# Kernel tuning notes

Hardware: AMD Instinct MI355X
Metric: run time of the kernel (lower is better)

The kernel has to match this reference:

```python
import jax, jax.numpy as jnp
import numpy as np

B, D, N, H = 1024, 512, 16, 512  # batch, latent, branches, hidden


def _lrelu(v):
    return jnp.where(v >= 0, v, 0.1 * v)  # LeakyReLU(0.1)


def setup_inputs() -> dict:
    key = jax.random.key(0)
    ks = jax.random.split(key, 9)
    s = 0.02
    return {
        "x": jax.random.normal(ks[0], (B, D, N), dtype=jnp.float32),
        "Ws1": jax.random.normal(ks[1], (D, D), dtype=jnp.float32) * s,
        "bs1": jnp.zeros((D,), dtype=jnp.float32),
        "Ws2": jax.random.normal(ks[2], (D, D), dtype=jnp.float32) * s,
        "bs2": jnp.zeros((D,), dtype=jnp.float32),
        # per-branch binary classifiers: Linear(D,H)+LeakyReLU+Linear(H,1)
        "Wc1": jax.random.normal(ks[3], (N, D, H), dtype=jnp.float32) * s,
        "bc1": jnp.zeros((N, H), dtype=jnp.float32),
        "Wc2": jax.random.normal(ks[4], (N, H), dtype=jnp.float32) * s,
        "bc2": jnp.zeros((N,), dtype=jnp.float32),
    }


def reference(x, Ws1, bs1, Ws2, bs2, Wc1, bc1, Wc2, bc2):
    # x: [B, D, N] -> per-branch tokens [B, N, D]
    xb = jnp.transpose(x, (0, 2, 1))
    # shared MLP applied to every branch slice (same weights)
    h = _lrelu(xb @ Ws1 + bs1)
    shared = _lrelu(h @ Ws2 + bs2)  # [B, N, D]
    # per-branch classifier on its own branch slice -> sigmoid probs
    h1 = _lrelu(jnp.einsum('bnd,ndh->bnh', shared, Wc1) + bc1)
    logits = jnp.einsum('bnh,nh->bn', h1, Wc2) + bc2  # [B, N]
    out = jax.nn.sigmoid(logits)[:, None, :]  # [B, 1, N]
    # full pass: concat branch slices along batch (branch-major), every
    # classifier applied to the full stack -> raw logits
    full_in = jnp.transpose(shared, (1, 0, 2)).reshape(N * B, D)  # [M, D]
    h2 = _lrelu(jnp.einsum('md,ndh->mnh', full_in, Wc1) + bc1)  # [M, N, H]
    full_logits = jnp.einsum('mnh,nh->mn', h2, Wc2) + bc2  # [M, N]
    full_out = full_logits[:, None, :]  # [N*B, 1, N]
    return (out, full_out)
```

## Files before the change

### kernel.cpp

```cpp
#include <hip/hip_runtime.h>
#include <hip/hip_bf16.h>
#include <stdint.h>

#define Bq 1024
#define Dq 512
#define Nq 16
#define Hq 512
#define Mq (Bq*Nq)

typedef short v8s  __attribute__((ext_vector_type(8)));
typedef float v16f __attribute__((ext_vector_type(16)));

typedef __attribute__((address_space(3))) unsigned int as3_u32;
typedef __attribute__((address_space(1))) const unsigned int as1_u32;

__device__ __forceinline__ unsigned short f2bf(float f) {
  union { float f; unsigned u; } v; v.f = f;
  return (unsigned short)((v.u + 0x7fffu + ((v.u >> 16) & 1u)) >> 16);
}

__global__ void k_transpose_x(const float* __restrict__ x, unsigned short* __restrict__ xb) {
  __shared__ float lds[Dq][Nq + 1];
  const int b = blockIdx.x;
  const float* xi = x + (size_t)b * Dq * Nq;
  const int t = threadIdx.x;
  for (int p = 0; p < (Dq*Nq)/256; ++p) {
    int i = t + p*256;
    lds[i >> 4][i & (Nq-1)] = xi[i];
  }
  __syncthreads();
  unsigned short* o = xb + (size_t)b * Nq * Dq;
  for (int p = 0; p < (Dq*Nq)/256; ++p) {
    int i = t + p*256;
    o[i] = f2bf(lds[i & (Dq-1)][i >> 9]);
  }
}

__global__ void k_transpose_w(const float* __restrict__ Ws1, const float* __restrict__ Ws2,
                              const float* __restrict__ Wc1,
                              unsigned short* __restrict__ Ws1t, unsigned short* __restrict__ Ws2t,
                              unsigned short* __restrict__ Wc1t) {
  __shared__ float tile[32][33];
  const int z = blockIdx.z;
  const float* in;
  unsigned short* out;
  if (z == 0)      { in = Ws1; out = Ws1t; }
  else if (z == 1) { in = Ws2; out = Ws2t; }
  else             { in = Wc1 + (size_t)(z-2) * 512 * 512; out = Wc1t + (size_t)(z-2) * 512 * 512; }
  const int tx = threadIdx.x, ty = threadIdx.y;
  const int c0 = blockIdx.x * 32, r0 = blockIdx.y * 32;
#pragma unroll
  for (int j = 0; j < 4; ++j)
    tile[ty + j*8][tx] = in[(size_t)(r0 + ty + j*8) * 512 + c0 + tx];
  __syncthreads();
#pragma unroll
  for (int j = 0; j < 4; ++j) {
    int c = c0 + ty + j*8;
    int r = r0 + tx;
    out[(size_t)c * 512 + r] = f2bf(tile[tx][ty + j*8]);
  }
}

template<int MODE, int BM>
__global__ __launch_bounds__(256, 2)
void k_gemm(const unsigned short* __restrict__ A,
            const unsigned short* __restrict__ Bt,
            const float* __restrict__ bias,
            void* __restrict__ out_,
            const float* __restrict__ w2,
            int permute) {
  constexpr int BN = 128, BK = 32, KD = 512;
  constexpr int NI = (BM == 256) ? 4 : 2;
  constexpr int AG = BM / 16;
  constexpr int TG = AG + BN / 16;
  __shared__ __align__(16) unsigned short As[2][BM][BK];
  __shared__ __align__(16) unsigned short Bs[2][BN][BK];

  const int t = threadIdx.x;
  const int wave = t >> 6, lane = t & 63;
  const int wr = (BM == 256) ? wave : (wave >> 1);
  const int wc = (BM == 256) ? 0    : (wave & 1);
  const int l32 = lane & 31, kh0 = lane >> 5;
  const int bm = blockIdx.x * BM, bn = blockIdx.y * BN;
  const int z = blockIdx.z;

  const unsigned short* Bz = Bt + (size_t)z * KD * 512;
  const float* biasz = bias + (size_t)z * 512;

  const int lrow = lane >> 2;
  const int lslot = lane & 3;

  auto stage = [&](int buf, int kt) {
#pragma unroll
    for (int i = wave; i < TG; i += 4) {
      const int isA = (i < AG);
      const int r0 = (isA ? i : i - AG) * 16;
      const int row = r0 + lrow;
      const int cg = lslot ^ ((row >> 1) & 3);
      const unsigned short* g = isA ? &A [(size_t)(bm + row) * KD + kt*BK + cg*8]
                                    : &Bz[(size_t)(bn + row) * KD + kt*BK + cg*8];
      as3_u32* d = isA ? (as3_u32*)&As[buf][r0][0] : (as3_u32*)&Bs[buf][r0][0];
      __builtin_amdgcn_global_load_lds((as1_u32*)g, d, 16, 0, 0);
    }
  };

  v16f acc[2][NI] = {};

  stage(0, 0);
  __syncthreads();

  for (int kt = 0; kt < KD / BK; ++kt) {
    const int cur = kt & 1;
    if (kt + 1 < KD / BK) stage(cur ^ 1, kt + 1);

    v8s af[2][2], bf[NI][2];
#pragma unroll
    for (int mi = 0; mi < 2; ++mi) {
      int ra = wr*64 + mi*32 + l32;
#pragma unroll
      for (int kh = 0; kh < 2; ++kh) {
        int c = kh*2 + kh0;
        af[mi][kh] = *(const v8s*)&As[cur][ra][(c ^ ((ra >> 1) & 3)) * 8];
      }
    }
#pragma unroll
    for (int ni = 0; ni < NI; ++ni) {
      int rb = wc*64 + ni*32 + l32;
#pragma unroll
      for (int kh = 0; kh < 2; ++kh) {
        int c = kh*2 + kh0;
        bf[ni][kh] = *(const v8s*)&Bs[cur][rb][(c ^ ((rb >> 1) & 3)) * 8];
      }
    }
#pragma unroll
    for (int kh = 0; kh < 2; ++kh)
#pragma unroll
      for (int mi = 0; mi < 2; ++mi)
#pragma unroll
        for (int ni = 0; ni < NI; ++ni)
          acc[mi][ni] = __builtin_amdgcn_mfma_f32_32x32x16_bf16(af[mi][kh], bf[ni][kh], acc[mi][ni], 0, 0, 0);
    __syncthreads();
  }

  if (MODE == 0) {
    unsigned short* O = (unsigned short*)out_;
#pragma unroll
    for (int mi = 0; mi < 2; ++mi) {
#pragma unroll
      for (int ni = 0; ni < NI; ++ni) {
        int col = bn + wc*64 + ni*32 + l32;
        float bcol = biasz[col];
#pragma unroll
        for (int reg = 0; reg < 16; ++reg) {
          int rl = (reg & 3) + 8*(reg >> 2) + 4*kh0;
          int grow = bm + wr*64 + mi*32 + rl;
          int orow = permute ? ((grow & 15) * Bq + (grow >> 4)) : grow;
          float v = acc[mi][ni][reg] + bcol;
          v = v >= 0.f ? v : 0.1f * v;
          O[(size_t)orow * 512 + col] = f2bf(v);
        }
      }
    }
  } else {
    float* FL = (float*)out_;
    const float* w2z = w2 + (size_t)z * 512;
#pragma unroll
    for (int mi = 0; mi < 2; ++mi) {
#pragma unroll
      for (int reg = 0; reg < 16; ++reg) {
        int rl = (reg & 3) + 8*(reg >> 2) + 4*kh0;
        float s = 0.f;
#pragma unroll
        for (int ni = 0; ni < NI; ++ni) {
          int col = bn + ni*32 + l32;
          float v = acc[mi][ni][reg] + biasz[col];
          v = v >= 0.f ? v : 0.1f * v;
          s += v * w2z[col];
        }
#pragma unroll
        for (int off = 1; off < 32; off <<= 1)
          s += __shfl_xor(s, off, 64);
        if (l32 == 0) {
          int grow = bm + wave*64 + mi*32 + rl;
          atomicAdd(&FL[(size_t)grow * Nq + z], s);
        }
      }
    }
  }
}

__global__ void k_final(const float* __restrict__ fl, const float* __restrict__ bc2,
                        float* __restrict__ out) {
  int i = blockIdx.x * 256 + threadIdx.x;
  int m = i >> 4, n = i & 15;
  float v = fl[i] + bc2[n];
  out[Mq + i] = v;
  if (n == (m >> 10)) {
    int b = m & (Bq - 1);
    out[b * Nq + n] = 1.f / (1.f + __expf(-v));
  }
}

extern "C" void kernel_launch(void* const* d_in, const int* in_sizes, int n_in,
                              void* d_out, int out_size, void* d_ws, size_t ws_size,
                              hipStream_t stream) {
  (void)in_sizes; (void)n_in; (void)out_size; (void)ws_size;
  const float* x   = (const float*)d_in[0];
  const float* Ws1 = (const float*)d_in[1];
  const float* bs1 = (const float*)d_in[2];
  const float* Ws2 = (const float*)d_in[3];
  const float* bs2 = (const float*)d_in[4];
  const float* Wc1 = (const float*)d_in[5];
  const float* bc1 = (const float*)d_in[6];
  const float* Wc2 = (const float*)d_in[7];
  const float* bc2 = (const float*)d_in[8];

  char* ws = (char*)d_ws;
  unsigned short* Xb   = (unsigned short*)(ws);
  unsigned short* Hbuf = (unsigned short*)(ws + (size_t)16*1024*1024);
  unsigned short* Sm   = (unsigned short*)(ws + (size_t)32*1024*1024);
  unsigned short* Ws1t = (unsigned short*)(ws + (size_t)48*1024*1024);
  unsigned short* Ws2t = (unsigned short*)(ws + (size_t)48*1024*1024 + 512*1024);
  unsigned short* Wc1t = (unsigned short*)(ws + (size_t)49*1024*1024);
  float*          FL   = (float*)         (ws + (size_t)57*1024*1024);

  hipMemsetAsync(FL, 0, (size_t)Mq * Nq * sizeof(float), stream);

  k_transpose_x<<<Bq, 256, 0, stream>>>(x, Xb);
  k_transpose_w<<<dim3(16,16,18), dim3(32,8), 0, stream>>>(Ws1, Ws2, Wc1, Ws1t, Ws2t, Wc1t);

  k_gemm<0,128><<<dim3(128,4,1), 256, 0, stream>>>(Xb,   Ws1t, bs1, Hbuf, nullptr, 0);
  k_gemm<0,128><<<dim3(128,4,1), 256, 0, stream>>>(Hbuf, Ws2t, bs2, Sm,   nullptr, 1);
  k_gemm<1,256><<<dim3(64,4,16), 256, 0, stream>>>(Sm, Wc1t, bc1, FL, Wc2, 0);

  k_final<<<(Mq*Nq)/256, 256, 0, stream>>>(FL, bc2, (float*)d_out);
}
```

Measured before the change: 342.4 us.

## Add 256x256 head GEMM kernel with 8 waves and fine-grained LDS pipelining

Replaces the dominant head GEMM (16 branches x 16384 rows x 512 x 512) with a new kernel that uses 512 threads and 256x256 output tiles. Global-to-LDS loads are split into half-K stages interleaved between MFMA groups, with explicit vmcnt waits, raw barriers, sched_barrier and s_setprio to keep loads in flight during compute. The larger tile halves the number of B-column blocks, so fewer atomics into FL and less operand refetch. The risks are higher register and LDS pressure (128 KB LDS with launch bounds of 2 blocks per CU) and fragile manual wait counts.

```diff
diff --git a/kernel.cpp b/kernel.cpp
--- a/kernel.cpp
+++ b/kernel.cpp
@@ -13,6 +13,8 @@
 
 typedef __attribute__((address_space(3))) unsigned int as3_u32;
 typedef __attribute__((address_space(1))) const unsigned int as1_u32;
+
+#define VMCNT(n) asm volatile("s_waitcnt vmcnt(" #n ")" ::: "memory")
 
 __device__ __forceinline__ unsigned short f2bf(float f) {
   union { float f; unsigned u; } v; v.f = f;
@@ -189,6 +191,136 @@
   }
 }
 
+__global__ __launch_bounds__(512, 2)
+void k_headgemm(const unsigned short* __restrict__ A,
+                const unsigned short* __restrict__ Bt,
+                const float* __restrict__ bias,
+                float* __restrict__ FL,
+                const float* __restrict__ w2) {
+  __shared__ __align__(16) unsigned short sm[2][2][2][256][32];
+
+  const int t = threadIdx.x;
+  const int wave = t >> 6, lane = t & 63;
+  const int wr = wave >> 2, wc = wave & 3;
+  const int l32 = lane & 31, kh0 = lane >> 5;
+  const int bm = blockIdx.x * 256, bn = blockIdx.y * 256;
+  const int z = blockIdx.z;
+
+  const unsigned short* Bz = Bt + (size_t)z * Dq * 512;
+  const float* biasz = bias + (size_t)z * 512;
+  const float* w2z   = w2   + (size_t)z * 512;
+
+  const int srow = wave*16 + (lane >> 2);
+  const int sgc  = (lane & 3) ^ ((srow >> 1) & 3);
+  const unsigned short* aSrc = A  + (size_t)(bm + srow) * Dq + sgc*8;
+  const unsigned short* bSrc = Bz + (size_t)(bn + srow) * Dq + sgc*8;
+
+  auto stageA = [&](int T, int h) {
+    const int buf = T & 1;
+    const unsigned short* g = aSrc + T*64 + h*32;
+#pragma unroll
+    for (int part = 0; part < 2; ++part) {
+      as3_u32* d = (as3_u32*)&sm[buf][h][0][part*128 + wave*16][0];
+      __builtin_amdgcn_global_load_lds((as1_u32*)(g + (size_t)part*128*Dq), d, 16, 0, 0);
+    }
+  };
+  auto stageB = [&](int T, int h) {
+    const int buf = T & 1;
+    const unsigned short* g = bSrc + T*64 + h*32;
+#pragma unroll
+    for (int part = 0; part < 2; ++part) {
+      as3_u32* d = (as3_u32*)&sm[buf][h][1][part*128 + wave*16][0];
+      __builtin_amdgcn_global_load_lds((as1_u32*)(g + (size_t)part*128*Dq), d, 16, 0, 0);
+    }
+  };
+
+  int offA[4][2], offB[2][2];
+#pragma unroll
+  for (int mi = 0; mi < 4; ++mi) {
+    int r = wr*128 + mi*32 + l32;
+#pragma unroll
+    for (int par = 0; par < 2; ++par)
+      offA[mi][par] = r*64 + (((par*2 + kh0) ^ ((r >> 1) & 3)) * 16);
+  }
+#pragma unroll
+  for (int ni = 0; ni < 2; ++ni) {
+    int r = wc*64 + ni*32 + l32;
+#pragma unroll
+    for (int par = 0; par < 2; ++par)
+      offB[ni][par] = r*64 + (((par*2 + kh0) ^ ((r >> 1) & 3)) * 16);
+  }
+
+  v16f acc[4][2] = {};
+
+  stageA(0, 0); stageB(0, 0);
+  stageA(0, 1); stageB(0, 1);
+  stageA(1, 0); stageB(1, 0);
+  VMCNT(8);
+  __builtin_amdgcn_s_barrier();
+
+  for (int tt = 0; tt < 8; ++tt) {
+    const int buf = tt & 1;
+#pragma unroll
+    for (int q = 0; q < 4; ++q) {
+      const int h = q >> 1, par = q & 1;
+      const char* baseA = (const char*)&sm[buf][h][0][0][0];
+      const char* baseB = (const char*)&sm[buf][h][1][0][0];
+      v8s af[4], bf[2];
+#pragma unroll
+      for (int mi = 0; mi < 4; ++mi) af[mi] = *(const v8s*)(baseA + offA[mi][par]);
+#pragma unroll
+      for (int ni = 0; ni < 2; ++ni) bf[ni] = *(const v8s*)(baseB + offB[ni][par]);
+
+      if      (q == 0) { if (tt + 1 < 8) stageA(tt + 1, 1); }
+      else if (q == 1) { if (tt + 1 < 8) stageB(tt + 1, 1); }
+      else if (q == 2) { if (tt + 2 < 8) stageA(tt + 2, 0); }
+      else             { if (tt + 2 < 8) stageB(tt + 2, 0); }
+
+      __builtin_amdgcn_s_barrier();
+
+      __builtin_amdgcn_s_setprio(1);
+#pragma unroll
+      for (int mi = 0; mi < 4; ++mi)
+#pragma unroll
+        for (int ni = 0; ni < 2; ++ni)
+          acc[mi][ni] = __builtin_amdgcn_mfma_f32_32x32x16_bf16(af[mi], bf[ni], acc[mi][ni], 0, 0, 0);
+      __builtin_amdgcn_s_setprio(0);
+
+      if (q == 1) {
+        if (tt < 7) { VMCNT(8); } else { VMCNT(0); }
+      } else if (q == 3) {
+        if (tt < 6)       { VMCNT(8); }
+        else if (tt == 6) { VMCNT(4); }
+      }
+      __builtin_amdgcn_s_barrier();
+      __builtin_amdgcn_sched_barrier(0);
+    }
+  }
+
+#pragma unroll
+  for (int mi = 0; mi < 4; ++mi) {
+#pragma unroll
+    for (int reg = 0; reg < 16; ++reg) {
+      int rl = (reg & 3) + 8*(reg >> 2) + 4*kh0;
+      float s = 0.f;
+#pragma unroll
+      for (int ni = 0; ni < 2; ++ni) {
+        int col = bn + wc*64 + ni*32 + l32;
+        float v = acc[mi][ni][reg] + biasz[col];
+        v = v >= 0.f ? v : 0.1f * v;
+        s += v * w2z[col];
+      }
+#pragma unroll
+      for (int off = 1; off < 32; off <<= 1)
+        s += __shfl_xor(s, off, 64);
+      if (l32 == 0) {
+        int grow = bm + wr*128 + mi*32 + rl;
+        atomicAdd(&FL[(size_t)grow * Nq + z], s);
+      }
+    }
+  }
+}
+
 __global__ void k_final(const float* __restrict__ fl, const float* __restrict__ bc2,
                         float* __restrict__ out) {
   int i = blockIdx.x * 256 + threadIdx.x;
@@ -231,7 +363,7 @@
 
   k_gemm<0,128><<<dim3(128,4,1), 256, 0, stream>>>(Xb,   Ws1t, bs1, Hbuf, nullptr, 0);
   k_gemm<0,128><<<dim3(128,4,1), 256, 0, stream>>>(Hbuf, Ws2t, bs2, Sm,   nullptr, 1);
-  k_gemm<1,256><<<dim3(64,4,16), 256, 0, stream>>>(Sm, Wc1t, bc1, FL, Wc2, 0);
+  k_headgemm<<<dim3(64,2,16), 512, 0, stream>>>(Sm, Wc1t, bc1, FL, Wc2);
 
   k_final<<<(Mq*Nq)/256, 256, 0, stream>>>(FL, bc2, (float*)d_out);
 }
```

New measurement: 405.9 us. 18.6% more time.

## Replace head GEMM with 256x256-tile 8-wave pipelined MFMA kernel

Applied to the files above, without the earlier changes.

Adds a dedicated head GEMM kernel with 256x256 output tiles, 512 threads and 16x16x32 bf16 MFMAs. It stages K in 64-wide double-buffered halves with direct global-to-LDS loads, manual vmcnt waits, s_barrier phases and setprio around MFMA bursts, so loads overlap compute. The larger tile halves the number of N-blocks, which reduces redundant A reads and atomic adds per row. In exchange it needs 128 KB of LDS per block and heavy accumulator register use, which may limit occupancy, and the hand-written sync is fragile.

```diff
diff --git a/kernel.cpp b/kernel.cpp
--- a/kernel.cpp
+++ b/kernel.cpp
@@ -9,10 +9,13 @@
 #define Mq (Bq*Nq)
 
 typedef short v8s  __attribute__((ext_vector_type(8)));
+typedef float v4f  __attribute__((ext_vector_type(4)));
 typedef float v16f __attribute__((ext_vector_type(16)));
 
 typedef __attribute__((address_space(3))) unsigned int as3_u32;
 typedef __attribute__((address_space(1))) const unsigned int as1_u32;
+
+#define VMCNT(n) asm volatile("s_waitcnt vmcnt(" #n ")" ::: "memory")
 
 __device__ __forceinline__ unsigned short f2bf(float f) {
   union { float f; unsigned u; } v; v.f = f;
@@ -189,6 +192,149 @@
   }
 }
 
+__global__ __launch_bounds__(512, 2)
+void k_headgemm(const unsigned short* __restrict__ A,
+                const unsigned short* __restrict__ Bt,
+                const float* __restrict__ bias,
+                float* __restrict__ FL,
+                const float* __restrict__ w2) {
+  __shared__ __align__(16) unsigned short sm[2][2][2][256][32];
+
+  const int t = threadIdx.x;
+  const int wave = t >> 6, lane = t & 63;
+  const int wr = wave >> 2, wc = wave & 3;
+  const int bm = blockIdx.x * 256, bn = blockIdx.y * 256;
+  const int z = blockIdx.z;
+
+  const unsigned short* Bz = Bt + (size_t)z * Dq * 512;
+  const float* biasz = bias + (size_t)z * 512;
+  const float* w2z   = w2   + (size_t)z * 512;
+
+  const int sr = lane >> 2;
+  const int sc = (lane & 3) ^ ((sr >> 1) & 3);
+  const unsigned short* aSrc = A  + (size_t)(bm + wave*32 + sr) * Dq + sc*8;
+  const unsigned short* bSrc = Bz + (size_t)(bn + wave*32 + sr) * Dq + sc*8;
+
+  auto stage = [&](int T, int h, int op) {
+    const unsigned short* src = (op == 0 ? aSrc : bSrc) + T*64 + h*32;
+#pragma unroll
+    for (int j = 0; j < 2; ++j) {
+      as3_u32* d = (as3_u32*)&sm[T & 1][h][op][wave*32 + j*16][0];
+      __builtin_amdgcn_global_load_lds((as1_u32*)(src + (size_t)j*16*Dq), d, 16, 0, 0);
+    }
+  };
+
+  const int fr = lane & 15, fq = lane >> 4;
+  const int swz = ((fq ^ ((fr >> 1) & 3)) * 16);
+  const int offA0 = (wr*128 + fr) * 64 + swz;
+  const int offB0 = (wc*64  + fr) * 64 + swz;
+
+  v4f acc[8][4] = {};
+
+  stage(0, 0, 0); stage(0, 0, 1);
+  stage(0, 1, 0); stage(0, 1, 1);
+  VMCNT(4);
+  __builtin_amdgcn_s_barrier();
+  __builtin_amdgcn_sched_barrier(0);
+
+#pragma unroll 2
+  for (int tt = 0; tt < 8; ++tt) {
+    const char* bA0 = (const char*)&sm[tt & 1][0][0][0][0];
+    const char* bB0 = (const char*)&sm[tt & 1][0][1][0][0];
+    const char* bA1 = (const char*)&sm[tt & 1][1][0][0][0];
+    const char* bB1 = (const char*)&sm[tt & 1][1][1][0][0];
+    v8s af[4], bf[4];
+
+#pragma unroll
+    for (int i = 0; i < 4; ++i) af[i] = *(const v8s*)(bA0 + offA0 + i*1024);
+#pragma unroll
+    for (int i = 0; i < 4; ++i) bf[i] = *(const v8s*)(bB0 + offB0 + i*1024);
+    if (tt + 1 < 8) stage(tt + 1, 0, 0);
+    __builtin_amdgcn_s_barrier();
+    __builtin_amdgcn_s_setprio(1);
+#pragma unroll
+    for (int mi = 0; mi < 4; ++mi)
+#pragma unroll
+      for (int ni = 0; ni < 4; ++ni)
+        acc[mi][ni] = __builtin_amdgcn_mfma_f32_16x16x32_bf16(af[mi], bf[ni], acc[mi][ni], 0, 0, 0);
+    __builtin_amdgcn_s_setprio(0);
+    __builtin_amdgcn_s_barrier();
+
+#pragma unroll
+    for (int i = 0; i < 4; ++i) af[i] = *(const v8s*)(bA0 + offA0 + (4 + i)*1024);
+    if (tt + 1 < 8) stage(tt + 1, 0, 1);
+    __builtin_amdgcn_s_barrier();
+    __builtin_amdgcn_s_setprio(1);
+#pragma unroll
+    for (int mi = 0; mi < 4; ++mi)
+#pragma unroll
+      for (int ni = 0; ni < 4; ++ni)
+        acc[4 + mi][ni] = __builtin_amdgcn_mfma_f32_16x16x32_bf16(af[mi], bf[ni], acc[4 + mi][ni], 0, 0, 0);
+    __builtin_amdgcn_s_setprio(0);
+    if (tt < 7) { VMCNT(4); } else { VMCNT(0); }
+    __builtin_amdgcn_s_barrier();
+    __builtin_amdgcn_sched_barrier(0);
+
+#pragma unroll
+    for (int i = 0; i < 4; ++i) af[i] = *(const v8s*)(bA1 + offA0 + i*1024);
+#pragma unroll
+    for (int i = 0; i < 4; ++i) bf[i] = *(const v8s*)(bB1 + offB0 + i*1024);
+    if (tt + 1 < 8) stage(tt + 1, 1, 0);
+    __builtin_amdgcn_s_barrier();
+    __builtin_amdgcn_s_setprio(1);
+#pragma unroll
+    for (int mi = 0; mi < 4; ++mi)
+#pragma unroll
+      for (int ni = 0; ni < 4; ++ni)
+        acc[mi][ni] = __builtin_amdgcn_mfma_f32_16x16x32_bf16(af[mi], bf[ni], acc[mi][ni], 0, 0, 0);
+    __builtin_amdgcn_s_setprio(0);
+    __builtin_amdgcn_s_barrier();
+
+#pragma unroll
+    for (int i = 0; i < 4; ++i) af[i] = *(const v8s*)(bA1 + offA0 + (4 + i)*1024);
+    if (tt + 1 < 8) stage(tt + 1, 1, 1);
+    __builtin_amdgcn_s_barrier();
+    __builtin_amdgcn_s_setprio(1);
+#pragma unroll
+    for (int mi = 0; mi < 4; ++mi)
+#pragma unroll
+      for (int ni = 0; ni < 4; ++ni)
+        acc[4 + mi][ni] = __builtin_amdgcn_mfma_f32_16x16x32_bf16(af[mi], bf[ni], acc[4 + mi][ni], 0, 0, 0);
+    __builtin_amdgcn_s_setprio(0);
+    if (tt < 7) { VMCNT(4); }
+    __builtin_amdgcn_s_barrier();
+    __builtin_amdgcn_sched_barrier(0);
+  }
+
+  float bcol[4], wcol[4];
+#pragma unroll
+  for (int ni = 0; ni < 4; ++ni) {
+    int col = bn + wc*64 + ni*16 + fr;
+    bcol[ni] = biasz[col];
+    wcol[ni] = w2z[col];
+  }
+#pragma unroll
+  for (int mi = 0; mi < 8; ++mi) {
+#pragma unroll
+    for (int reg = 0; reg < 4; ++reg) {
+      float s = 0.f;
+#pragma unroll
+      for (int ni = 0; ni < 4; ++ni) {
+        float v = acc[mi][ni][reg] + bcol[ni];
+        v = v >= 0.f ? v : 0.1f * v;
+        s += v * wcol[ni];
+      }
+#pragma unroll
+      for (int off = 1; off < 16; off <<= 1)
+        s += __shfl_xor(s, off, 64);
+      if (fr == 0) {
+        int grow = bm + wr*128 + mi*16 + fq*4 + reg;
+        atomicAdd(&FL[(size_t)grow * Nq + z], s);
+      }
+    }
+  }
+}
+
 __global__ void k_final(const float* __restrict__ fl, const float* __restrict__ bc2,
                         float* __restrict__ out) {
   int i = blockIdx.x * 256 + threadIdx.x;
@@ -231,7 +377,7 @@
 
   k_gemm<0,128><<<dim3(128,4,1), 256, 0, stream>>>(Xb,   Ws1t, bs1, Hbuf, nullptr, 0);
   k_gemm<0,128><<<dim3(128,4,1), 256, 0, stream>>>(Hbuf, Ws2t, bs2, Sm,   nullptr, 1);
-  k_gemm<1,256><<<dim3(64,4,16), 256, 0, stream>>>(Sm, Wc1t, bc1, FL, Wc2, 0);
+  k_headgemm<<<dim3(64,2,16), 512, 0, stream>>>(Sm, Wc1t, bc1, FL, Wc2);
 
   k_final<<<(Mq*Nq)/256, 256, 0, stream>>>(FL, bc2, (float*)d_out);
 }
```

New measurement: 334.5 us. -2.3%, faster.

## Replace head GEMM with triple-buffered 16x16 MFMA kernel and XCD-aware block mapping

Applied to the files above, without the earlier changes.

Adds a dedicated kernel for the dominant per-branch head GEMM. It uses 128x128 tiles, a three-stage LDS ring filled by global_load_lds with explicit vmcnt waits and raw s_barrier, 16x16x32 bf16 MFMA with a 4x4 per-wave fragment, and s_setprio around the MFMA block. Blocks are linearised with a stride-8 remap so blocks that share weight and activation tiles land on the same XCD. The goal is to hide global latency better and raise occupancy compared with the double-buffered 256-row kernel. In exchange it issues more atomicAdds per output row, and the hand-placed wait counts must stay exactly right.

```diff
diff --git a/kernel.cpp b/kernel.cpp
--- a/kernel.cpp
+++ b/kernel.cpp
@@ -9,10 +9,13 @@
 #define Mq (Bq*Nq)
 
 typedef short v8s  __attribute__((ext_vector_type(8)));
+typedef float v4f  __attribute__((ext_vector_type(4)));
 typedef float v16f __attribute__((ext_vector_type(16)));
 
 typedef __attribute__((address_space(3))) unsigned int as3_u32;
 typedef __attribute__((address_space(1))) const unsigned int as1_u32;
+
+#define VMCNT(n) asm volatile("s_waitcnt vmcnt(" #n ")" ::: "memory")
 
 __device__ __forceinline__ unsigned short f2bf(float f) {
   union { float f; unsigned u; } v; v.f = f;
@@ -189,6 +192,122 @@
   }
 }
 
+__global__ __launch_bounds__(256, 3)
+void k_headgemm(const unsigned short* __restrict__ A,
+                const unsigned short* __restrict__ Bt,
+                const float* __restrict__ bias,
+                float* __restrict__ FL,
+                const float* __restrict__ w2) {
+  __shared__ __align__(16) unsigned short As[3][128][32];
+  __shared__ __align__(16) unsigned short Bs[3][128][32];
+
+  const int t = threadIdx.x;
+  const int wave = t >> 6, lane = t & 63;
+  const int wr = wave >> 1, wc = wave & 1;
+  const int fr = lane & 15, fq = lane >> 4;
+
+  const int bid = blockIdx.x;
+  const int lin = (bid & 7) * 1024 + (bid >> 3);
+  const int bm = (lin & 127) * 128;
+  const int bn = ((lin >> 7) & 3) * 128;
+  const int z  = lin >> 9;
+
+  const unsigned short* Bz = Bt + (size_t)z * Dq * 512;
+  const float* biasz = bias + (size_t)z * 512;
+  const float* w2z   = w2   + (size_t)z * 512;
+
+  const int sr = lane >> 2;
+  const int sc = (lane & 3) ^ ((sr >> 1) & 3);
+  const unsigned short* aSrc = A  + (size_t)(bm + wave*32 + sr) * Dq + sc*8;
+  const unsigned short* bSrc = Bz + (size_t)(bn + wave*32 + sr) * Dq + sc*8;
+  char* dstA = (char*)As + (wave*32) * 64;
+  char* dstB = (char*)Bs + (wave*32) * 64;
+
+  auto stage = [&](int T, int slot) {
+    if (T >= 16) return;
+#pragma unroll
+    for (int j = 0; j < 2; ++j) {
+      __builtin_amdgcn_global_load_lds((as1_u32*)(aSrc + T*32 + (size_t)j*16*Dq),
+                                       (as3_u32*)(dstA + slot*8192 + j*1024), 16, 0, 0);
+      __builtin_amdgcn_global_load_lds((as1_u32*)(bSrc + T*32 + (size_t)j*16*Dq),
+                                       (as3_u32*)(dstB + slot*8192 + j*1024), 16, 0, 0);
+    }
+  };
+
+  const int swz = (fq ^ ((fr >> 1) & 3)) * 16;
+  int offA[4], offB[4];
+#pragma unroll
+  for (int mi = 0; mi < 4; ++mi) offA[mi] = (wr*64 + mi*16 + fr) * 64 + swz;
+#pragma unroll
+  for (int ni = 0; ni < 4; ++ni) offB[ni] = (wc*64 + ni*16 + fr) * 64 + swz;
+
+  v4f acc[4][4] = {};
+
+  stage(0, 0);
+  stage(1, 1);
+  VMCNT(4);
+  __builtin_amdgcn_s_barrier();
+  __builtin_amdgcn_sched_barrier(0);
+
+  int sR = 0, sS = 2;
+  for (int kt = 0; kt < 16; ++kt) {
+    stage(kt + 2, sS);
+
+    const char* aB = (const char*)As + sR * 8192;
+    const char* bB = (const char*)Bs + sR * 8192;
+    v8s af[4], bf[4];
+#pragma unroll
+    for (int i = 0; i < 4; ++i) af[i] = *(const v8s*)(aB + offA[i]);
+#pragma unroll
+    for (int i = 0; i < 4; ++i) bf[i] = *(const v8s*)(bB + offB[i]);
+
+    __builtin_amdgcn_s_setprio(1);
+#pragma unroll
+    for (int mi = 0; mi < 4; ++mi)
+#pragma unroll
+      for (int ni = 0; ni < 4; ++ni)
+        acc[mi][ni] = __builtin_amdgcn_mfma_f32_16x16x32_bf16(af[mi], bf[ni], acc[mi][ni], 0, 0, 0);
+    __builtin_amdgcn_s_setprio(0);
+
+    if (kt < 14)       { VMCNT(4); }
+    else if (kt == 14) { VMCNT(0); }
+    if (kt < 15) {
+      __builtin_amdgcn_s_barrier();
+      __builtin_amdgcn_sched_barrier(0);
+    }
+    sR = (sR + 1 == 3) ? 0 : sR + 1;
+    sS = (sS + 1 == 3) ? 0 : sS + 1;
+  }
+
+  float bcol[4], wcol[4];
+#pragma unroll
+  for (int ni = 0; ni < 4; ++ni) {
+    int col = bn + wc*64 + ni*16 + fr;
+    bcol[ni] = biasz[col];
+    wcol[ni] = w2z[col];
+  }
+#pragma unroll
+  for (int mi = 0; mi < 4; ++mi) {
+#pragma unroll
+    for (int reg = 0; reg < 4; ++reg) {
+      float s = 0.f;
+#pragma unroll
+      for (int ni = 0; ni < 4; ++ni) {
+        float v = acc[mi][ni][reg] + bcol[ni];
+        v = v >= 0.f ? v : 0.1f * v;
+        s += v * wcol[ni];
+      }
+#pragma unroll
+      for (int off = 1; off < 16; off <<= 1)
+        s += __shfl_xor(s, off, 64);
+      if (fr == 0) {
+        int grow = bm + wr*64 + mi*16 + fq*4 + reg;
+        atomicAdd(&FL[(size_t)grow * Nq + z], s);
+      }
+    }
+  }
+}
+
 __global__ void k_final(const float* __restrict__ fl, const float* __restrict__ bc2,
                         float* __restrict__ out) {
   int i = blockIdx.x * 256 + threadIdx.x;
@@ -231,7 +350,7 @@
 
   k_gemm<0,128><<<dim3(128,4,1), 256, 0, stream>>>(Xb,   Ws1t, bs1, Hbuf, nullptr, 0);
   k_gemm<0,128><<<dim3(128,4,1), 256, 0, stream>>>(Hbuf, Ws2t, bs2, Sm,   nullptr, 1);
-  k_gemm<1,256><<<dim3(64,4,16), 256, 0, stream>>>(Sm, Wc1t, bc1, FL, Wc2, 0);
+  k_headgemm<<<8192, 256, 0, stream>>>(Sm, Wc1t, bc1, FL, Wc2);
 
   k_final<<<(Mq*Nq)/256, 256, 0, stream>>>(FL, bc2, (float*)d_out);
 }
```

Measured after the change: 351.2 us. 1.03x slower.
